# Optimization experiments

Measured on AMD Instinct MI355X. Metric: run time of the kernel, lower is better.

The kernel has to match this reference:

```python
import jax, jax.numpy as jnp
import numpy as np

IN_F = 512
OUT_F = 512

def setup_inputs() -> dict:
    key = jax.random.key(0)
    k1, k2, k3 = jax.random.split(key, 3)
    x = jax.random.normal(k1, (2, 512, IN_F), dtype=jnp.float32)
    # uniform init: a = sqrt(6 / (2 + out_features))
    a = float(np.sqrt(6.0 / (2.0 + OUT_F)))
    W = jax.random.uniform(k2, (OUT_F, IN_F), dtype=jnp.float32, minval=-a, maxval=a)
    bound = float(1.0 / np.sqrt(IN_F))
    b = jax.random.uniform(k3, (OUT_F,), dtype=jnp.float32, minval=-bound, maxval=bound)
    return {"x": x, "W": W, "b": b}

def reference(x, W, b):
    # MAM fully connected (beta == 0 path): for each (row, out-neuron),
    # C = max_k(x_k * w_ok) + min_k(x_k * w_ok), then add bias.
    xf = x.reshape(-1, x.shape[-1])            # (B, in)
    prod = xf[:, None, :] * W[None, :, :]      # (B, out, in) -- the large intermediate
    C = prod.max(axis=-1) + prod.min(axis=-1)  # (B, out)
    C = C + b[None, :]
    return C.reshape(x.shape[:-1] + (W.shape[0],))
```

## Files before the change

kernel.cpp:

```cpp
#include <hip/hip_runtime.h>
#include <math.h>


#define K_TOTAL 512
#define O_TOTAL 512
#define OW 64
#define RPB 8
#define NSEG 8
#define KSEG (K_TOTAL / NSEG)

__global__ __launch_bounds__(256)
void transpose_w(const float* __restrict__ W, float* __restrict__ WT) {
  __shared__ float tile[64][65];
  const int t = threadIdx.x;
  const int ob = blockIdx.x & 7;
  const int kb = blockIdx.x >> 3;
  const int o0 = ob * 64, k0 = kb * 64;
#pragma unroll
  for (int i = 0; i < 4; ++i) {
    const int u = t + 256 * i, r = u >> 4, c = u & 15;
    const float4 v = *reinterpret_cast<const float4*>(W + (size_t)(o0 + r) * K_TOTAL + k0 + c * 4);
    tile[r][c * 4 + 0] = v.x; tile[r][c * 4 + 1] = v.y;
    tile[r][c * 4 + 2] = v.z; tile[r][c * 4 + 3] = v.w;
  }
  __syncthreads();
#pragma unroll
  for (int i = 0; i < 4; ++i) {
    const int u = t + 256 * i, kr = u >> 4, c = u & 15;
    float4 v;
    v.x = tile[c * 4 + 0][kr]; v.y = tile[c * 4 + 1][kr];
    v.z = tile[c * 4 + 2][kr]; v.w = tile[c * 4 + 3][kr];
    *reinterpret_cast<float4*>(WT + (size_t)(k0 + kr) * O_TOTAL + o0 + c * 4) = v;
  }
}

template <bool TRANS>
__global__ __launch_bounds__(512, 8)
void mam_fc_kernel(const float* __restrict__ x, const float* __restrict__ Wm,
                   const float* __restrict__ bias, float* __restrict__ out) {
  __shared__ float red[NSEG][RPB][OW][2];

  const int t = threadIdx.x;
  const int lane = t & 63;
  const int q = __builtin_amdgcn_readfirstlane(t >> 6);
  const int ob = blockIdx.x & 7;
  const int rg = blockIdx.x >> 3;
  const int o0 = ob * OW;
  const int row0 = rg * RPB;
  const int k0 = q * KSEG;

  const float* xb = x + (size_t)row0 * K_TOTAL + k0;

  float amax[RPB], amin[RPB];
#pragma unroll
  for (int r = 0; r < RPB; ++r) { amax[r] = -INFINITY; amin[r] = INFINITY; }

#pragma unroll 4
  for (int kk = 0; kk < KSEG; kk += 2) {
    float wa, wb;
    if (TRANS) {
      wa = Wm[(size_t)(k0 + kk) * O_TOTAL + o0 + lane];
      wb = Wm[(size_t)(k0 + kk + 1) * O_TOTAL + o0 + lane];
    } else {
      wa = Wm[(size_t)(o0 + lane) * K_TOTAL + k0 + kk];
      wb = Wm[(size_t)(o0 + lane) * K_TOTAL + k0 + kk + 1];
    }
#pragma unroll
    for (int r = 0; r < RPB; ++r) {
      const float xa = xb[(size_t)r * K_TOTAL + kk];
      const float xc = xb[(size_t)r * K_TOTAL + kk + 1];
      const float pa = xa * wa;
      const float pb = xc * wb;
      amax[r] = fmaxf(fmaxf(amax[r], pa), pb);
      amin[r] = fminf(fminf(amin[r], pa), pb);
    }
  }

#pragma unroll
  for (int r = 0; r < RPB; ++r) {
    red[q][r][lane][0] = amax[r];
    red[q][r][lane][1] = amin[r];
  }
  __syncthreads();

  const int rr = t >> 6;
  const int oo = t & 63;
  float m = -INFINITY, n = INFINITY;
#pragma unroll
  for (int s = 0; s < NSEG; ++s) {
    m = fmaxf(m, red[s][rr][oo][0]);
    n = fminf(n, red[s][rr][oo][1]);
  }
  out[(size_t)(row0 + rr) * O_TOTAL + o0 + oo] = m + n + bias[o0 + oo];
}

extern "C" void kernel_launch(void* const* d_in, const int* in_sizes, int n_in,
                              void* d_out, int out_size, void* d_ws, size_t ws_size,
                              hipStream_t stream) {
  const float* x = (const float*)d_in[0];
  const float* W = (const float*)d_in[1];
  const float* b = (const float*)d_in[2];
  float* out = (float*)d_out;

  const int nrows = in_sizes[0] / K_TOTAL;
  const int nblocks = (O_TOTAL / OW) * (nrows / RPB);
  const size_t wt_bytes = (size_t)K_TOTAL * O_TOTAL * sizeof(float);

  if (ws_size >= wt_bytes) {
    float* WT = (float*)d_ws;
    transpose_w<<<dim3(64), dim3(256), 0, stream>>>(W, WT);
    mam_fc_kernel<true><<<dim3(nblocks), dim3(512), 0, stream>>>(x, WT, b, out);
  } else {
    mam_fc_kernel<false><<<dim3(nblocks), dim3(512), 0, stream>>>(x, W, b, out);
  }
}
```

Baseline: 24.44 us.

## Halve K-split to 4 waves and vectorize x loads as float4

Reduces the block from 512 to 256 threads by splitting K into 4 segments instead of 8, so each wave processes 128 k values. x loads become float4 per row, using an asm zero-VGPR trick to force vector loads instead of scalar ones. The cross-segment reduction shrinks and each thread now produces two outputs. This gives more ILP per wave and fewer loads per product, at the cost of fewer waves in flight and a longer per-wave serial chain.

Result: slower. 44.96 us (+83.9%).

```diff
diff --git a/kernel.cpp b/kernel.cpp
--- a/kernel.cpp
+++ b/kernel.cpp
@@ -6,8 +6,8 @@
 #define O_TOTAL 512
 #define OW 64
 #define RPB 8
-#define NSEG 8
-#define KSEG (K_TOTAL / NSEG)
+#define NQ 4
+#define KQ (K_TOTAL / NQ)
 
 __global__ __launch_bounds__(256)
 void transpose_w(const float* __restrict__ W, float* __restrict__ WT) {
@@ -35,10 +35,10 @@
 }
 
 template <bool TRANS>
-__global__ __launch_bounds__(512, 8)
+__global__ __launch_bounds__(256, 4)
 void mam_fc_kernel(const float* __restrict__ x, const float* __restrict__ Wm,
                    const float* __restrict__ bias, float* __restrict__ out) {
-  __shared__ float red[NSEG][RPB][OW][2];
+  __shared__ float red[NQ][RPB][OW][2];
 
   const int t = threadIdx.x;
   const int lane = t & 63;
@@ -47,32 +47,40 @@
   const int rg = blockIdx.x >> 3;
   const int o0 = ob * OW;
   const int row0 = rg * RPB;
-  const int k0 = q * KSEG;
+  const int k0 = q * KQ;
 
-  const float* xb = x + (size_t)row0 * K_TOTAL + k0;
+  int vzero;
+  asm("v_mov_b32 %0, 0" : "=v"(vzero));
+  const float* xrow[RPB];
+#pragma unroll
+  for (int r = 0; r < RPB; ++r)
+    xrow[r] = x + (size_t)(row0 + r) * K_TOTAL + k0 + vzero;
 
   float amax[RPB], amin[RPB];
 #pragma unroll
   for (int r = 0; r < RPB; ++r) { amax[r] = -INFINITY; amin[r] = INFINITY; }
 
-#pragma unroll 4
-  for (int kk = 0; kk < KSEG; kk += 2) {
-    float wa, wb;
+#pragma unroll 2
+  for (int kk = 0; kk < KQ; kk += 4) {
+    float w0, w1, w2, w3;
     if (TRANS) {
-      wa = Wm[(size_t)(k0 + kk) * O_TOTAL + o0 + lane];
-      wb = Wm[(size_t)(k0 + kk + 1) * O_TOTAL + o0 + lane];
+      w0 = Wm[(size_t)(k0 + kk + 0) * O_TOTAL + o0 + lane];
+      w1 = Wm[(size_t)(k0 + kk + 1) * O_TOTAL + o0 + lane];
+      w2 = Wm[(size_t)(k0 + kk + 2) * O_TOTAL + o0 + lane];
+      w3 = Wm[(size_t)(k0 + kk + 3) * O_TOTAL + o0 + lane];
     } else {
-      wa = Wm[(size_t)(o0 + lane) * K_TOTAL + k0 + kk];
-      wb = Wm[(size_t)(o0 + lane) * K_TOTAL + k0 + kk + 1];
+      const float* wr = Wm + (size_t)(o0 + lane) * K_TOTAL + k0 + kk;
+      w0 = wr[0]; w1 = wr[1]; w2 = wr[2]; w3 = wr[3];
     }
 #pragma unroll
     for (int r = 0; r < RPB; ++r) {
-      const float xa = xb[(size_t)r * K_TOTAL + kk];
-      const float xc = xb[(size_t)r * K_TOTAL + kk + 1];
-      const float pa = xa * wa;
-      const float pb = xc * wb;
-      amax[r] = fmaxf(fmaxf(amax[r], pa), pb);
-      amin[r] = fminf(fminf(amin[r], pa), pb);
+      const float4 xv = *reinterpret_cast<const float4*>(xrow[r] + kk);
+      const float p0 = xv.x * w0;
+      const float p1 = xv.y * w1;
+      const float p2 = xv.z * w2;
+      const float p3 = xv.w * w3;
+      amax[r] = fmaxf(fmaxf(fmaxf(fmaxf(amax[r], p0), p1), p2), p3);
+      amin[r] = fminf(fminf(fminf(fminf(amin[r], p0), p1), p2), p3);
     }
   }
 
@@ -83,15 +91,18 @@
   }
   __syncthreads();
 
-  const int rr = t >> 6;
-  const int oo = t & 63;
-  float m = -INFINITY, n = INFINITY;
 #pragma unroll
-  for (int s = 0; s < NSEG; ++s) {
-    m = fmaxf(m, red[s][rr][oo][0]);
-    n = fminf(n, red[s][rr][oo][1]);
+  for (int i = 0; i < 2; ++i) {
+    const int idx = t + 256 * i;
+    const int rr = idx >> 6, oo = idx & 63;
+    float m = red[0][rr][oo][0], n = red[0][rr][oo][1];
+#pragma unroll
+    for (int s = 1; s < NQ; ++s) {
+      m = fmaxf(m, red[s][rr][oo][0]);
+      n = fminf(n, red[s][rr][oo][1]);
+    }
+    out[(size_t)(row0 + rr) * O_TOTAL + o0 + oo] = m + n + bias[o0 + oo];
   }
-  out[(size_t)(row0 + rr) * O_TOTAL + o0 + oo] = m + n + bias[o0 + oo];
 }
 
 extern "C" void kernel_launch(void* const* d_in, const int* in_sizes, int n_in,
@@ -109,8 +120,8 @@
   if (ws_size >= wt_bytes) {
     float* WT = (float*)d_ws;
     transpose_w<<<dim3(64), dim3(256), 0, stream>>>(W, WT);
-    mam_fc_kernel<true><<<dim3(nblocks), dim3(512), 0, stream>>>(x, WT, b, out);
+    mam_fc_kernel<true><<<dim3(nblocks), dim3(256), 0, stream>>>(x, WT, b, out);
   } else {
-    mam_fc_kernel<false><<<dim3(nblocks), dim3(512), 0, stream>>>(x, W, b, out);
+    mam_fc_kernel<false><<<dim3(nblocks), dim3(256), 0, stream>>>(x, W, b, out);
   }
 }
```

## Compute MAM products and max/min in packed fp16 with pre-converted inputs

Applied to the files above, without the earlier changes.

Adds kernels that convert W (transposed, pair-packed) and x into half2 buffers, then runs the main max/min reduction with packed fp16 multiply, max and min over k-pairs. This halves the number of vector instructions and the bytes loaded in the hot loop. It adds an extra kernel launch for converting x and lowers numerical precision of the products to fp16. The no-workspace fallback is replaced by a simple naive kernel.

Measured after the change: 30.61 us. 1.25x slower.

```diff
diff --git a/kernel.cpp b/kernel.cpp
--- a/kernel.cpp
+++ b/kernel.cpp
@@ -2,41 +2,35 @@
 #include <math.h>
 
 
+typedef _Float16 h2 __attribute__((ext_vector_type(2)));
+
 #define K_TOTAL 512
 #define O_TOTAL 512
+#define KP_TOTAL 256
 #define OW 64
 #define RPB 8
 #define NSEG 8
-#define KSEG (K_TOTAL / NSEG)
+#define KPSEG (KP_TOTAL / NSEG)
 
 __global__ __launch_bounds__(256)
-void transpose_w(const float* __restrict__ W, float* __restrict__ WT) {
-  __shared__ float tile[64][65];
-  const int t = threadIdx.x;
-  const int ob = blockIdx.x & 7;
-  const int kb = blockIdx.x >> 3;
-  const int o0 = ob * 64, k0 = kb * 64;
-#pragma unroll
-  for (int i = 0; i < 4; ++i) {
-    const int u = t + 256 * i, r = u >> 4, c = u & 15;
-    const float4 v = *reinterpret_cast<const float4*>(W + (size_t)(o0 + r) * K_TOTAL + k0 + c * 4);
-    tile[r][c * 4 + 0] = v.x; tile[r][c * 4 + 1] = v.y;
-    tile[r][c * 4 + 2] = v.z; tile[r][c * 4 + 3] = v.w;
-  }
-  __syncthreads();
-#pragma unroll
-  for (int i = 0; i < 4; ++i) {
-    const int u = t + 256 * i, kr = u >> 4, c = u & 15;
-    float4 v;
-    v.x = tile[c * 4 + 0][kr]; v.y = tile[c * 4 + 1][kr];
-    v.z = tile[c * 4 + 2][kr]; v.w = tile[c * 4 + 3][kr];
-    *reinterpret_cast<float4*>(WT + (size_t)(k0 + kr) * O_TOTAL + o0 + c * 4) = v;
-  }
+void conv_w(const float* __restrict__ W, h2* __restrict__ WP) {
+  const int tid = blockIdx.x * 256 + threadIdx.x;
+  const int o = tid >> 8;
+  const int kp = tid & 255;
+  const float2 v = *reinterpret_cast<const float2*>(W + (size_t)o * K_TOTAL + kp * 2);
+  WP[(size_t)kp * O_TOTAL + o] = h2{(_Float16)v.x, (_Float16)v.y};
 }
 
-template <bool TRANS>
+__global__ __launch_bounds__(256)
+void conv_x(const float* __restrict__ x, h2* __restrict__ XH, int total) {
+  const int tid = blockIdx.x * 256 + threadIdx.x;
+  if (tid >= total) return;
+  const float2 v = *reinterpret_cast<const float2*>(x + (size_t)tid * 2);
+  XH[tid] = h2{(_Float16)v.x, (_Float16)v.y};
+}
+
 __global__ __launch_bounds__(512, 8)
-void mam_fc_kernel(const float* __restrict__ x, const float* __restrict__ Wm,
+void mam_fc_kernel(const h2* __restrict__ XH, const h2* __restrict__ WP,
                    const float* __restrict__ bias, float* __restrict__ out) {
   __shared__ float red[NSEG][RPB][OW][2];
 
@@ -47,51 +41,62 @@
   const int rg = blockIdx.x >> 3;
   const int o0 = ob * OW;
   const int row0 = rg * RPB;
-  const int k0 = q * KSEG;
+  const int kp0 = q * KPSEG;
 
-  const float* xb = x + (size_t)row0 * K_TOTAL + k0;
+  const h2* xb = XH + (size_t)row0 * KP_TOTAL + kp0;
+  const h2* wb = WP + (size_t)kp0 * O_TOTAL + o0 + lane;
 
-  float amax[RPB], amin[RPB];
+  h2 amax[RPB], amin[RPB];
 #pragma unroll
-  for (int r = 0; r < RPB; ++r) { amax[r] = -INFINITY; amin[r] = INFINITY; }
+  for (int r = 0; r < RPB; ++r) {
+    amax[r] = h2{(_Float16)(-65504.f), (_Float16)(-65504.f)};
+    amin[r] = h2{(_Float16)(65504.f), (_Float16)(65504.f)};
+  }
 
 #pragma unroll 4
-  for (int kk = 0; kk < KSEG; kk += 2) {
-    float wa, wb;
-    if (TRANS) {
-      wa = Wm[(size_t)(k0 + kk) * O_TOTAL + o0 + lane];
-      wb = Wm[(size_t)(k0 + kk + 1) * O_TOTAL + o0 + lane];
-    } else {
-      wa = Wm[(size_t)(o0 + lane) * K_TOTAL + k0 + kk];
-      wb = Wm[(size_t)(o0 + lane) * K_TOTAL + k0 + kk + 1];
-    }
+  for (int kp = 0; kp < KPSEG; ++kp) {
+    const h2 w2 = wb[(size_t)kp * O_TOTAL];
 #pragma unroll
     for (int r = 0; r < RPB; ++r) {
-      const float xa = xb[(size_t)r * K_TOTAL + kk];
-      const float xc = xb[(size_t)r * K_TOTAL + kk + 1];
-      const float pa = xa * wa;
-      const float pb = xc * wb;
-      amax[r] = fmaxf(fmaxf(amax[r], pa), pb);
-      amin[r] = fminf(fminf(amin[r], pa), pb);
+      const h2 x2 = xb[(size_t)r * KP_TOTAL + kp];
+      const h2 p = x2 * w2;
+      amax[r] = __builtin_elementwise_max(amax[r], p);
+      amin[r] = __builtin_elementwise_min(amin[r], p);
     }
   }
 
 #pragma unroll
   for (int r = 0; r < RPB; ++r) {
-    red[q][r][lane][0] = amax[r];
-    red[q][r][lane][1] = amin[r];
+    red[q][r][lane][0] = fmaxf((float)amax[r][0], (float)amax[r][1]);
+    red[q][r][lane][1] = fminf((float)amin[r][0], (float)amin[r][1]);
   }
   __syncthreads();
 
   const int rr = t >> 6;
   const int oo = t & 63;
-  float m = -INFINITY, n = INFINITY;
+  float m = red[0][rr][oo][0], n = red[0][rr][oo][1];
 #pragma unroll
-  for (int s = 0; s < NSEG; ++s) {
+  for (int s = 1; s < NSEG; ++s) {
     m = fmaxf(m, red[s][rr][oo][0]);
     n = fminf(n, red[s][rr][oo][1]);
   }
   out[(size_t)(row0 + rr) * O_TOTAL + o0 + oo] = m + n + bias[o0 + oo];
+}
+
+__global__ __launch_bounds__(256)
+void mam_fc_fallback(const float* __restrict__ x, const float* __restrict__ W,
+                     const float* __restrict__ bias, float* __restrict__ out,
+                     int nrows) {
+  const int idx = blockIdx.x * 256 + threadIdx.x;
+  if (idx >= nrows * O_TOTAL) return;
+  const int r = idx >> 9, o = idx & 511;
+  float m = -INFINITY, n = INFINITY;
+  for (int k = 0; k < K_TOTAL; ++k) {
+    const float p = x[(size_t)r * K_TOTAL + k] * W[(size_t)o * K_TOTAL + k];
+    m = fmaxf(m, p);
+    n = fminf(n, p);
+  }
+  out[idx] = m + n + bias[o];
 }
 
 extern "C" void kernel_launch(void* const* d_in, const int* in_sizes, int n_in,
@@ -103,14 +108,20 @@
   float* out = (float*)d_out;
 
   const int nrows = in_sizes[0] / K_TOTAL;
-  const int nblocks = (O_TOTAL / OW) * (nrows / RPB);
-  const size_t wt_bytes = (size_t)K_TOTAL * O_TOTAL * sizeof(float);
+  const int xh_elems = nrows * KP_TOTAL;
+  const size_t wp_bytes = (size_t)KP_TOTAL * O_TOTAL * sizeof(h2);
+  const size_t xh_bytes = (size_t)xh_elems * sizeof(h2);
 
-  if (ws_size >= wt_bytes) {
-    float* WT = (float*)d_ws;
-    transpose_w<<<dim3(64), dim3(256), 0, stream>>>(W, WT);
-    mam_fc_kernel<true><<<dim3(nblocks), dim3(512), 0, stream>>>(x, WT, b, out);
+  if (ws_size >= wp_bytes + xh_bytes) {
+    h2* WP = (h2*)d_ws;
+    h2* XH = (h2*)((char*)d_ws + wp_bytes);
+    conv_w<<<dim3(512), dim3(256), 0, stream>>>(W, WP);
+    conv_x<<<dim3((xh_elems + 255) / 256), dim3(256), 0, stream>>>(x, XH, xh_elems);
+    const int nblocks = (O_TOTAL / OW) * (nrows / RPB);
+    mam_fc_kernel<<<dim3(nblocks), dim3(512), 0, stream>>>(XH, WP, b, out);
   } else {
-    mam_fc_kernel<false><<<dim3(nblocks), dim3(512), 0, stream>>>(x, W, b, out);
+    const int nthreads = nrows * O_TOTAL;
+    mam_fc_fallback<<<dim3((nthreads + 255) / 256), dim3(256), 0, stream>>>(
+        x, W, b, out, nrows);
   }
 }
```
